# Kernel optimization log

Measured on AMD Instinct MI355X. Metric: run time of the kernel, lower is better.

## Reference

```python
import jax, jax.numpy as jnp
import numpy as np

RADIUS = [1.0, 1.5, 2.0, 100.0]  # bucket boundaries; last is catch-all
NFILT = len(RADIUS)
C_IN, C_OUT = 256, 512


def setup_inputs() -> dict:
    key = jax.random.key(0)
    k1, k2, k3, k4 = jax.random.split(key, 4)
    b, n = 16, 4096
    feat = jax.random.normal(k1, (b, n, C_IN), dtype=jnp.float32)
    xyz = jax.random.normal(k2, (b, n, 3), dtype=jnp.float32)
    # init per original reset_parameters
    std = 2.0 * np.sqrt(2.0 / (C_IN + C_OUT))
    a = np.sqrt(3.0) * std
    weight = jax.random.uniform(k3, (NFILT, C_OUT, C_IN), dtype=jnp.float32, minval=-a, maxval=a)
    bound = 1.0 / np.sqrt(C_IN)
    bias = jax.random.uniform(k4, (NFILT, C_OUT), dtype=jnp.float32, minval=-bound, maxval=bound)
    return {"feat": feat, "xyz": xyz, "weight": weight, "bias": bias}


def reference(feat, xyz, weight, bias):
    b, n, c = feat.shape
    p = feat.reshape(b * n, c)                      # (P, C)
    radii = jnp.asarray(RADIUS, dtype=feat.dtype)
    r_norm = jnp.linalg.norm(xyz.reshape(b * n, 3), axis=1)
    # first radius with r_norm < r (same as the sequential break in map2filtId)
    filt_id = jnp.argmax(r_norm[:, None] < radii[None, :], axis=1)  # (P,)
    # grouped linear expressed densely: all Nfilt GEMMs, then per-point select
    all_out = jnp.einsum('pc,foc->fpo', p, weight) + bias[:, None, :]  # (F, P, O)
    out = jnp.take_along_axis(all_out, filt_id[None, :, None], axis=0)[0]  # (P, O)
    return out.reshape(b, n, -1)
```

## Files before the change

### kernel.cpp

```cpp
#include <hip/hip_runtime.h>
#include <hip/hip_bf16.h>

#define C_IN   256
#define C_OUT  512
#define NFILT  4

#define BM 128
#define BN 128
#define BK 32
#define SAS 40

typedef __attribute__((ext_vector_type(8))) short bf16x8;
typedef __attribute__((ext_vector_type(4))) float floatx4;

union Pack8 { uint4 u; __hip_bfloat16 h[8]; };

__global__ void zero_cnt_kernel(int* __restrict__ cnt) {
    if (threadIdx.x < NFILT) cnt[threadIdx.x] = 0;
}

__global__ void bucketize_kernel(const float* __restrict__ xyz,
                                 int* __restrict__ idxbuf,
                                 int* __restrict__ cnt, int P) {
    int pid = blockIdx.x * blockDim.x + threadIdx.x;
    if (pid >= P) return;
    float x = xyz[pid * 3 + 0];
    float y = xyz[pid * 3 + 1];
    float z = xyz[pid * 3 + 2];
    float r2 = __fadd_rn(__fadd_rn(__fmul_rn(x, x), __fmul_rn(y, y)), __fmul_rn(z, z));
    float r = sqrtf(r2);
    int filt;
    if (r < 1.0f)        filt = 0;
    else if (r < 1.5f)   filt = 1;
    else if (r < 2.0f)   filt = 2;
    else if (r < 100.0f) filt = 3;
    else                 filt = 0;

    int lane = threadIdx.x & 63;
    for (int f = 0; f < NFILT; ++f) {
        unsigned long long mask = __ballot(filt == f);
        if (mask == 0ull) continue;
        int leader = __ffsll((unsigned long long)mask) - 1;
        int base = 0;
        if (lane == leader) base = atomicAdd(&cnt[f], __popcll(mask));
        base = __shfl(base, leader);
        if (filt == f) {
            int off = __popcll(mask & ((1ull << lane) - 1ull));
            idxbuf[f * P + base + off] = pid;
        }
    }
}

__global__ void convert_w_kernel(const float* __restrict__ w,
                                 ushort* __restrict__ wb) {
    int i = (blockIdx.x * blockDim.x + threadIdx.x) * 4;
    float4 v = *(const float4*)(w + i);
    union { ushort4 u; __hip_bfloat16 h[4]; } cv;
    cv.h[0] = __float2bfloat16(v.x);
    cv.h[1] = __float2bfloat16(v.y);
    cv.h[2] = __float2bfloat16(v.z);
    cv.h[3] = __float2bfloat16(v.w);
    *(ushort4*)(wb + i) = cv.u;
}

__global__ __launch_bounds__(256) void gemm_kernel(
    const float* __restrict__ feat, const ushort* __restrict__ wb,
    const float* __restrict__ bias, const int* __restrict__ idxbuf,
    const int* __restrict__ cnt, float* __restrict__ out, int P)
{
    __shared__ ushort sA[BM * SAS];
    __shared__ ushort sB[BN * SAS];
    __shared__ int    sIdx[BM];
    __shared__ float  sBias[BN];

    int t = blockIdx.y;
    int counts[4];
    counts[0] = cnt[0]; counts[1] = cnt[1]; counts[2] = cnt[2]; counts[3] = cnt[3];
    int f = -1, lt = 0;
    for (int ff = 0; ff < 4; ++ff) {
        int nt = (counts[ff] + BM - 1) / BM;
        if (t < nt) { f = ff; lt = t; break; }
        t -= nt;
    }
    if (f < 0) return;

    int tid = threadIdx.x;
    int oBase = blockIdx.x * BN;
    int rowBase = lt * BM;
    int cn = counts[f];

    if (tid < BM) {
        int r = rowBase + tid;
        sIdx[tid] = (r < cn) ? idxbuf[f * P + r] : -1;
    }
    if (tid < BN) sBias[tid] = bias[f * C_OUT + oBase + tid];
    __syncthreads();

    int sRow = tid >> 1;
    int sHalf = tid & 1;
    int myIdx = sIdx[sRow];
    const float* aRow = feat + (size_t)(myIdx < 0 ? 0 : myIdx) * C_IN + sHalf * 16;
    const ushort* bRow = wb + (size_t)(f * C_OUT + oBase + sRow) * C_IN + sHalf * 16;

    int wid = tid >> 6;
    int lane = tid & 63;
    int wm = (wid >> 1) * 64;
    int wn = (wid & 1) * 64;
    int lcol = lane & 15;
    int quad = lane >> 4;

    floatx4 acc[4][4];
#pragma unroll
    for (int i = 0; i < 4; ++i)
#pragma unroll
        for (int j = 0; j < 4; ++j)
            acc[i][j] = (floatx4){0.f, 0.f, 0.f, 0.f};

    for (int kk = 0; kk < C_IN; kk += BK) {
        const float* ap = aRow + kk;
        float4 a0 = *(const float4*)(ap + 0);
        float4 a1 = *(const float4*)(ap + 4);
        float4 a2 = *(const float4*)(ap + 8);
        float4 a3 = *(const float4*)(ap + 12);
        const ushort* bp = bRow + kk;
        uint4 b01 = *(const uint4*)(bp + 0);
        uint4 b23 = *(const uint4*)(bp + 8);

        Pack8 p0, p1;
        p0.h[0] = __float2bfloat16(a0.x); p0.h[1] = __float2bfloat16(a0.y);
        p0.h[2] = __float2bfloat16(a0.z); p0.h[3] = __float2bfloat16(a0.w);
        p0.h[4] = __float2bfloat16(a1.x); p0.h[5] = __float2bfloat16(a1.y);
        p0.h[6] = __float2bfloat16(a1.z); p0.h[7] = __float2bfloat16(a1.w);
        p1.h[0] = __float2bfloat16(a2.x); p1.h[1] = __float2bfloat16(a2.y);
        p1.h[2] = __float2bfloat16(a2.z); p1.h[3] = __float2bfloat16(a2.w);
        p1.h[4] = __float2bfloat16(a3.x); p1.h[5] = __float2bfloat16(a3.y);
        p1.h[6] = __float2bfloat16(a3.z); p1.h[7] = __float2bfloat16(a3.w);

        ushort* dA = &sA[sRow * SAS + sHalf * 16];
        *(uint4*)(dA + 0) = p0.u;
        *(uint4*)(dA + 8) = p1.u;
        ushort* dB = &sB[sRow * SAS + sHalf * 16];
        *(uint4*)(dB + 0) = b01;
        *(uint4*)(dB + 8) = b23;

        __syncthreads();

        bf16x8 af[4], bfr[4];
#pragma unroll
        for (int i = 0; i < 4; ++i)
            af[i] = *(const bf16x8*)&sA[(wm + i * 16 + lcol) * SAS + quad * 8];
#pragma unroll
        for (int j = 0; j < 4; ++j)
            bfr[j] = *(const bf16x8*)&sB[(wn + j * 16 + lcol) * SAS + quad * 8];
#pragma unroll
        for (int i = 0; i < 4; ++i)
#pragma unroll
            for (int j = 0; j < 4; ++j)
                acc[i][j] = __builtin_amdgcn_mfma_f32_16x16x32_bf16(af[i], bfr[j], acc[i][j], 0, 0, 0);

        __syncthreads();
    }

#pragma unroll
    for (int i = 0; i < 4; ++i) {
        int r0 = wm + i * 16 + quad * 4;
        int pid0 = sIdx[r0 + 0];
        int pid1 = sIdx[r0 + 1];
        int pid2 = sIdx[r0 + 2];
        int pid3 = sIdx[r0 + 3];
#pragma unroll
        for (int j = 0; j < 4; ++j) {
            int o = oBase + wn + j * 16 + lcol;
            float bv = sBias[wn + j * 16 + lcol];
            if (pid0 >= 0) out[pid0 * C_OUT + o] = acc[i][j][0] + bv;
            if (pid1 >= 0) out[pid1 * C_OUT + o] = acc[i][j][1] + bv;
            if (pid2 >= 0) out[pid2 * C_OUT + o] = acc[i][j][2] + bv;
            if (pid3 >= 0) out[pid3 * C_OUT + o] = acc[i][j][3] + bv;
        }
    }
}

extern "C" void kernel_launch(void* const* d_in, const int* in_sizes, int n_in,
                              void* d_out, int out_size, void* d_ws, size_t ws_size,
                              hipStream_t stream) {
    const float* feat = (const float*)d_in[0];
    const float* xyz  = (const float*)d_in[1];
    const float* w    = (const float*)d_in[2];
    const float* bias = (const float*)d_in[3];
    float* out = (float*)d_out;
    int P = in_sizes[0] / C_IN;

    char* ws = (char*)d_ws;
    int* idxbuf = (int*)ws;
    int* cntp   = (int*)(ws + (size_t)4 * P * 4);
    ushort* wb  = (ushort*)(ws + (size_t)4 * P * 4 + 16);

    zero_cnt_kernel<<<1, 64, 0, stream>>>(cntp);
    bucketize_kernel<<<(P + 255) / 256, 256, 0, stream>>>(xyz, idxbuf, cntp, P);
    convert_w_kernel<<<(NFILT * C_OUT * C_IN) / 1024, 256, 0, stream>>>(w, wb);

    dim3 grid(C_OUT / BN, P / BM + NFILT);
    gemm_kernel<<<grid, 256, 0, stream>>>(feat, wb, bias, idxbuf, cntp, out, P);
}
```

Baseline: 275.6 us.

## Load full A row-tile once, stream pre-swizzled B from global across all outputs

Each block now handles 128 gathered rows across all 512 outputs. It converts the full 256-wide A tile to bf16 in LDS once, instead of once for each of four column blocks. Weights are pre-laid out in an MFMA-fragment-friendly transposed order so B fragments load straight from global/L2 with register double-buffering. The change also removes the per-k-step barriers and uses nontemporal loads and stores. The tradeoffs are much larger LDS (about 66KB) and fewer blocks, and B comes from L2 rather than shared memory.

New measurement: 285.8 us. +3.7%, slower.

```diff
diff --git a/kernel.cpp b/kernel.cpp
--- a/kernel.cpp
+++ b/kernel.cpp
@@ -5,13 +5,12 @@
 #define C_OUT  512
 #define NFILT  4
 
-#define BM 128
-#define BN 128
-#define BK 32
-#define SAS 40
+#define BM  128
+#define SAS 264
 
 typedef __attribute__((ext_vector_type(8))) short bf16x8;
 typedef __attribute__((ext_vector_type(4))) float floatx4;
+typedef __attribute__((ext_vector_type(4))) float f4v;
 
 union Pack8 { uint4 u; __hip_bfloat16 h[8]; };
 
@@ -52,80 +51,63 @@
 }
 
 __global__ void convert_w_kernel(const float* __restrict__ w,
-                                 ushort* __restrict__ wb) {
-    int i = (blockIdx.x * blockDim.x + threadIdx.x) * 4;
-    float4 v = *(const float4*)(w + i);
-    union { ushort4 u; __hip_bfloat16 h[4]; } cv;
-    cv.h[0] = __float2bfloat16(v.x);
-    cv.h[1] = __float2bfloat16(v.y);
-    cv.h[2] = __float2bfloat16(v.z);
-    cv.h[3] = __float2bfloat16(v.w);
-    *(ushort4*)(wb + i) = cv.u;
-}
-
-__global__ __launch_bounds__(256) void gemm_kernel(
-    const float* __restrict__ feat, const ushort* __restrict__ wb,
+                                 ushort* __restrict__ wbt) {
+    int t = blockIdx.x * blockDim.x + threadIdx.x;
+    int c8 = t & 31;
+    int fo = t >> 5;
+    int f  = fo >> 9;
+    int o  = fo & 511;
+    const float* src = w + (size_t)fo * C_IN + c8 * 8;
+    f4v v0 = *(const f4v*)(src + 0);
+    f4v v1 = *(const f4v*)(src + 4);
+    Pack8 p;
+    p.h[0] = __float2bfloat16(v0.x); p.h[1] = __float2bfloat16(v0.y);
+    p.h[2] = __float2bfloat16(v0.z); p.h[3] = __float2bfloat16(v0.w);
+    p.h[4] = __float2bfloat16(v1.x); p.h[5] = __float2bfloat16(v1.y);
+    p.h[6] = __float2bfloat16(v1.z); p.h[7] = __float2bfloat16(v1.w);
+    *(uint4*)(wbt + ((size_t)(f * 32 + c8) * 512 + o) * 8) = p.u;
+}
+
+__global__ __launch_bounds__(256, 2) void gemm_kernel(
+    const float* __restrict__ feat, const ushort* __restrict__ wbt,
     const float* __restrict__ bias, const int* __restrict__ idxbuf,
     const int* __restrict__ cnt, float* __restrict__ out, int P)
 {
     __shared__ ushort sA[BM * SAS];
-    __shared__ ushort sB[BN * SAS];
+    __shared__ float  sBias[C_OUT];
     __shared__ int    sIdx[BM];
-    __shared__ float  sBias[BN];
-
-    int t = blockIdx.y;
-    int counts[4];
-    counts[0] = cnt[0]; counts[1] = cnt[1]; counts[2] = cnt[2]; counts[3] = cnt[3];
-    int f = -1, lt = 0;
-    for (int ff = 0; ff < 4; ++ff) {
-        int nt = (counts[ff] + BM - 1) / BM;
-        if (t < nt) { f = ff; lt = t; break; }
+
+    int t = blockIdx.x;
+    int f = -1, lt = 0, cn = 0;
+    for (int ff = 0; ff < NFILT; ++ff) {
+        int c = cnt[ff];
+        int nt = (c + BM - 1) / BM;
+        if (t < nt) { f = ff; lt = t; cn = c; break; }
         t -= nt;
     }
     if (f < 0) return;
 
     int tid = threadIdx.x;
-    int oBase = blockIdx.x * BN;
     int rowBase = lt * BM;
-    int cn = counts[f];
-
     if (tid < BM) {
         int r = rowBase + tid;
         sIdx[tid] = (r < cn) ? idxbuf[f * P + r] : -1;
     }
-    if (tid < BN) sBias[tid] = bias[f * C_OUT + oBase + tid];
+    sBias[tid]       = bias[f * C_OUT + tid];
+    sBias[tid + 256] = bias[f * C_OUT + tid + 256];
     __syncthreads();
 
-    int sRow = tid >> 1;
-    int sHalf = tid & 1;
+    int sRow = tid >> 1, sHalf = tid & 1;
     int myIdx = sIdx[sRow];
     const float* aRow = feat + (size_t)(myIdx < 0 ? 0 : myIdx) * C_IN + sHalf * 16;
-    const ushort* bRow = wb + (size_t)(f * C_OUT + oBase + sRow) * C_IN + sHalf * 16;
-
-    int wid = tid >> 6;
-    int lane = tid & 63;
-    int wm = (wid >> 1) * 64;
-    int wn = (wid & 1) * 64;
-    int lcol = lane & 15;
-    int quad = lane >> 4;
-
-    floatx4 acc[4][4];
-#pragma unroll
-    for (int i = 0; i < 4; ++i)
-#pragma unroll
-        for (int j = 0; j < 4; ++j)
-            acc[i][j] = (floatx4){0.f, 0.f, 0.f, 0.f};
-
-    for (int kk = 0; kk < C_IN; kk += BK) {
-        const float* ap = aRow + kk;
-        float4 a0 = *(const float4*)(ap + 0);
-        float4 a1 = *(const float4*)(ap + 4);
-        float4 a2 = *(const float4*)(ap + 8);
-        float4 a3 = *(const float4*)(ap + 12);
-        const ushort* bp = bRow + kk;
-        uint4 b01 = *(const uint4*)(bp + 0);
-        uint4 b23 = *(const uint4*)(bp + 8);
-
+    ushort* dA = &sA[sRow * SAS + sHalf * 16];
+#pragma unroll
+    for (int it = 0; it < 8; ++it) {
+        const float* ap = aRow + it * 32;
+        f4v a0 = __builtin_nontemporal_load((const f4v*)(ap + 0));
+        f4v a1 = __builtin_nontemporal_load((const f4v*)(ap + 4));
+        f4v a2 = __builtin_nontemporal_load((const f4v*)(ap + 8));
+        f4v a3 = __builtin_nontemporal_load((const f4v*)(ap + 12));
         Pack8 p0, p1;
         p0.h[0] = __float2bfloat16(a0.x); p0.h[1] = __float2bfloat16(a0.y);
         p0.h[2] = __float2bfloat16(a0.z); p0.h[3] = __float2bfloat16(a0.w);
@@ -135,47 +117,77 @@
         p1.h[2] = __float2bfloat16(a2.z); p1.h[3] = __float2bfloat16(a2.w);
         p1.h[4] = __float2bfloat16(a3.x); p1.h[5] = __float2bfloat16(a3.y);
         p1.h[6] = __float2bfloat16(a3.z); p1.h[7] = __float2bfloat16(a3.w);
-
-        ushort* dA = &sA[sRow * SAS + sHalf * 16];
-        *(uint4*)(dA + 0) = p0.u;
-        *(uint4*)(dA + 8) = p1.u;
-        ushort* dB = &sB[sRow * SAS + sHalf * 16];
-        *(uint4*)(dB + 0) = b01;
-        *(uint4*)(dB + 8) = b23;
-
-        __syncthreads();
-
-        bf16x8 af[4], bfr[4];
-#pragma unroll
-        for (int i = 0; i < 4; ++i)
-            af[i] = *(const bf16x8*)&sA[(wm + i * 16 + lcol) * SAS + quad * 8];
-#pragma unroll
-        for (int j = 0; j < 4; ++j)
-            bfr[j] = *(const bf16x8*)&sB[(wn + j * 16 + lcol) * SAS + quad * 8];
-#pragma unroll
-        for (int i = 0; i < 4; ++i)
-#pragma unroll
-            for (int j = 0; j < 4; ++j)
-                acc[i][j] = __builtin_amdgcn_mfma_f32_16x16x32_bf16(af[i], bfr[j], acc[i][j], 0, 0, 0);
-
-        __syncthreads();
-    }
-
-#pragma unroll
-    for (int i = 0; i < 4; ++i) {
-        int r0 = wm + i * 16 + quad * 4;
-        int pid0 = sIdx[r0 + 0];
-        int pid1 = sIdx[r0 + 1];
-        int pid2 = sIdx[r0 + 2];
-        int pid3 = sIdx[r0 + 3];
-#pragma unroll
-        for (int j = 0; j < 4; ++j) {
-            int o = oBase + wn + j * 16 + lcol;
-            float bv = sBias[wn + j * 16 + lcol];
-            if (pid0 >= 0) out[pid0 * C_OUT + o] = acc[i][j][0] + bv;
-            if (pid1 >= 0) out[pid1 * C_OUT + o] = acc[i][j][1] + bv;
-            if (pid2 >= 0) out[pid2 * C_OUT + o] = acc[i][j][2] + bv;
-            if (pid3 >= 0) out[pid3 * C_OUT + o] = acc[i][j][3] + bv;
+        *(uint4*)(dA + it * 32 + 0) = p0.u;
+        *(uint4*)(dA + it * 32 + 8) = p1.u;
+    }
+    __syncthreads();
+
+    int wid = tid >> 6, lane = tid & 63;
+    int lcol = lane & 15, quad = lane >> 4;
+    int rbase = wid * 32;
+    int aOff0 = (rbase + lcol) * SAS + quad * 8;
+    int aOff1 = aOff0 + 16 * SAS;
+
+    int    pid_[2][4];
+    size_t obase_[2][4];
+#pragma unroll
+    for (int i = 0; i < 2; ++i)
+#pragma unroll
+        for (int r = 0; r < 4; ++r) {
+            int p_ = sIdx[rbase + i * 16 + quad * 4 + r];
+            pid_[i][r]   = p_;
+            obase_[i][r] = (size_t)(p_ < 0 ? 0 : p_) * C_OUT + lcol;
+        }
+
+    const ushort* bQuad = wbt + ((size_t)(f * 32 + quad) * 512 + lcol) * 8;
+
+    for (int ot = 0; ot < 4; ++ot) {
+        floatx4 acc[2][8];
+#pragma unroll
+        for (int i = 0; i < 2; ++i)
+#pragma unroll
+            for (int j = 0; j < 8; ++j)
+                acc[i][j] = (floatx4){0.f, 0.f, 0.f, 0.f};
+
+        const ushort* bOt = bQuad + (size_t)ot * 128 * 8;
+
+        bf16x8 af[2][2], bfr[2][8];
+        af[0][0] = *(const bf16x8*)&sA[aOff0];
+        af[0][1] = *(const bf16x8*)&sA[aOff1];
+#pragma unroll
+        for (int j = 0; j < 8; ++j)
+            bfr[0][j] = *(const bf16x8*)(bOt + j * 16 * 8);
+
+#pragma unroll
+        for (int kk = 0; kk < 8; ++kk) {
+            int cur = kk & 1, nxt = cur ^ 1;
+            if (kk < 7) {
+                af[nxt][0] = *(const bf16x8*)&sA[aOff0 + (kk + 1) * 32];
+                af[nxt][1] = *(const bf16x8*)&sA[aOff1 + (kk + 1) * 32];
+                const ushort* bp = bOt + (size_t)(kk + 1) * 4 * 512 * 8;
+#pragma unroll
+                for (int j = 0; j < 8; ++j)
+                    bfr[nxt][j] = *(const bf16x8*)(bp + j * 16 * 8);
+            }
+#pragma unroll
+            for (int i = 0; i < 2; ++i)
+#pragma unroll
+                for (int j = 0; j < 8; ++j)
+                    acc[i][j] = __builtin_amdgcn_mfma_f32_16x16x32_bf16(
+                        af[cur][i], bfr[cur][j], acc[i][j], 0, 0, 0);
+        }
+
+#pragma unroll
+        for (int j = 0; j < 8; ++j) {
+            float bv = sBias[ot * 128 + j * 16 + lcol];
+#pragma unroll
+            for (int i = 0; i < 2; ++i)
+#pragma unroll
+                for (int r = 0; r < 4; ++r) {
+                    if (pid_[i][r] >= 0)
+                        __builtin_nontemporal_store(acc[i][j][r] + bv,
+                            out + obase_[i][r] + ot * 128 + j * 16);
+                }
         }
     }
 }
@@ -193,12 +205,12 @@
     char* ws = (char*)d_ws;
     int* idxbuf = (int*)ws;
     int* cntp   = (int*)(ws + (size_t)4 * P * 4);
-    ushort* wb  = (ushort*)(ws + (size_t)4 * P * 4 + 16);
+    ushort* wbt = (ushort*)(ws + (size_t)4 * P * 4 + 16);
 
     zero_cnt_kernel<<<1, 64, 0, stream>>>(cntp);
     bucketize_kernel<<<(P + 255) / 256, 256, 0, stream>>>(xyz, idxbuf, cntp, P);
-    convert_w_kernel<<<(NFILT * C_OUT * C_IN) / 1024, 256, 0, stream>>>(w, wb);
-
-    dim3 grid(C_OUT / BN, P / BM + NFILT);
-    gemm_kernel<<<grid, 256, 0, stream>>>(feat, wb, bias, idxbuf, cntp, out, P);
-}
+    convert_w_kernel<<<(NFILT * C_OUT * C_IN / 8 + 255) / 256, 256, 0, stream>>>(w, wbt);
+
+    dim3 grid(P / BM + NFILT);
+    gemm_kernel<<<grid, 256, 0, stream>>>(feat, wbt, bias, idxbuf, cntp, out, P);
+}
```
